# Kernel optimization log

Measured on AMD Instinct MI355X. Metric: run time of the kernel, lower is better.

The kernel has to match this reference:

```python
import jax, jax.numpy as jnp
import numpy as np

INPUT_DIM = 1024
EMBED_DIM = 1024
NUM_HEADS = 16
HEAD_DIM = EMBED_DIM // NUM_HEADS


def _xavier_uniform(key, shape):
    fan_in, fan_out = shape[1], shape[0]
    limit = float(np.sqrt(6.0 / (fan_in + fan_out)))
    return jax.random.uniform(key, shape, jnp.float32, -limit, limit)


def setup_inputs() -> dict:
    key = jax.random.key(0)
    kx, kqkv, ko = jax.random.split(key, 3)
    return {
        "x": jax.random.normal(kx, (2, 2048, INPUT_DIM), jnp.float32),
        "qkv_w": _xavier_uniform(kqkv, (3 * EMBED_DIM, INPUT_DIM)),
        "qkv_b": jnp.zeros((3 * EMBED_DIM,), jnp.float32),
        "o_w": _xavier_uniform(ko, (EMBED_DIM, INPUT_DIM)),
        "o_b": jnp.zeros((EMBED_DIM,), jnp.float32),
    }


def reference(x, qkv_w, qkv_b, o_w, o_b):
    B, S, _ = x.shape
    scale = HEAD_DIM ** -0.5
    # fused QKV projection: [B,S,3E]
    qkv = jnp.einsum('bsd,ed->bse', x, qkv_w) + qkv_b
    # [B,S,H,3Dh] -> [B,H,S,3Dh], then split into q,k,v
    qkv = qkv.reshape(B, S, NUM_HEADS, 3 * HEAD_DIM).transpose(0, 2, 1, 3)
    q, k, v = jnp.split(qkv, 3, axis=-1)
    # scaled dot-product attention
    scores = jnp.einsum('bhqd,bhkd->bhqk', q, k) * scale
    attn = jax.nn.softmax(scores, axis=-1)
    values = jnp.einsum('bhqk,bhkd->bhqd', attn, v)
    # [B,H,S,Dh] -> [B,S,E]
    values = values.transpose(0, 2, 1, 3).reshape(B, S, EMBED_DIM)
    return jnp.einsum('bse,oe->bso', values, o_w) + o_b
```

## Files before the change

### kernel.cpp

```cpp
#include <hip/hip_runtime.h>
#include <hip/hip_bf16.h>

typedef __bf16  bf16x8 __attribute__((ext_vector_type(8)));
typedef __bf16  bf16x4 __attribute__((ext_vector_type(4)));
typedef float   f32x4  __attribute__((ext_vector_type(4)));

#define LOG2E 1.44269504088896340736f

__device__ __forceinline__ void async_copy16(const void* g, void* l) {
  __builtin_amdgcn_global_load_lds(
      (const __attribute__((address_space(1))) unsigned int*)g,
      (__attribute__((address_space(3))) unsigned int*)l, 16, 0, 0);
}

#define C0 524288
#define C1 393216
#define C2 384
#define C3 131072
#define C4 128
#define CTOT (C0 + C1 + C2 + C3 + C4)
__global__ void convert_all(const void* __restrict__ x,  const void* __restrict__ qw,
                            const void* __restrict__ qb, const void* __restrict__ ow,
                            const void* __restrict__ ob,
                            __bf16* __restrict__ cx,  __bf16* __restrict__ cqw,
                            __bf16* __restrict__ cqb, __bf16* __restrict__ cow,
                            __bf16* __restrict__ cob, int* __restrict__ flag) {
  __shared__ int cnt;
  if (threadIdx.x == 0) cnt = 0;
  __syncthreads();
  unsigned int w = ((const unsigned int*)qw)[threadIdx.x];
  if (w & 0x4000u) atomicAdd(&cnt, 1);
  __syncthreads();
  const int f = (cnt > 16) ? 1 : 0;
  if (threadIdx.x == 0) *flag = f;

  int i = blockIdx.x * blockDim.x + threadIdx.x;
  const int stride = gridDim.x * blockDim.x;
  for (; i < CTOT; i += stride) {
    const void* s; __bf16* d; int off;
    if      (i < C0)                { s = x;  d = cx;  off = i; }
    else if (i < C0 + C1)           { s = qw; d = cqw; off = i - C0; }
    else if (i < C0 + C1 + C2)      { s = qb; d = cqb; off = i - C0 - C1; }
    else if (i < C0 + C1 + C2 + C3) { s = ow; d = cow; off = i - C0 - C1 - C2; }
    else                            { s = ob; d = cob; off = i - C0 - C1 - C2 - C3; }
    if (f) {
      const f32x4* sp = (const f32x4*)s;
      f32x4 a = sp[2 * off], b = sp[2 * off + 1];
      bf16x8 o;
      o[0] = (__bf16)a[0]; o[1] = (__bf16)a[1]; o[2] = (__bf16)a[2]; o[3] = (__bf16)a[3];
      o[4] = (__bf16)b[0]; o[5] = (__bf16)b[1]; o[6] = (__bf16)b[2]; o[7] = (__bf16)b[3];
      *(bf16x8*)&d[8 * off] = o;
    } else {
      *(bf16x8*)&d[8 * off] = ((const bf16x8*)s)[off];
    }
  }
}

template<int BN>
__global__ __launch_bounds__(256) void gemm_nt_bias(
    const __bf16* __restrict__ A,
    const __bf16* __restrict__ Bt,
    const __bf16* __restrict__ bias,
    __bf16* __restrict__ Cb,
    float* __restrict__ Cf,
    __bf16* __restrict__ vt,
    const int* __restrict__ flag,
    int M, int N, int K)
{
  constexpr int NI  = BN / 32;
  constexpr int NIB = BN / 32;
  __shared__ __align__(16) __bf16 As[128 * 64];
  __shared__ __align__(16) __bf16 Bs[BN * 64];

  const int tid  = threadIdx.x;
  const int lane = tid & 63;
  const int wave = tid >> 6;
  const int qd   = lane >> 4;
  const int ln   = lane & 15;
  const int m0 = blockIdx.y * 128;
  const int n0 = blockIdx.x * BN;
  const int wm = (wave >> 1) * 64;
  const int wn = (wave & 1) * (16 * NI);

  f32x4 acc[4][NI] = {};

  for (int kt = 0; kt < K; kt += 64) {
#pragma unroll
    for (int i = 0; i < 4; ++i) {
      int s = wave * 256 + i * 64 + lane;
      int r = s >> 3;
      int c = (s & 7) ^ (r & 7);
      async_copy16(A + (size_t)(m0 + r) * K + kt + c * 8, &As[(wave * 256 + i * 64) * 8]);
    }
#pragma unroll
    for (int i = 0; i < NIB; ++i) {
      int s = wave * (64 * NIB) + i * 64 + lane;
      int r = s >> 3;
      int c = (s & 7) ^ (r & 7);
      async_copy16(Bt + (size_t)(n0 + r) * K + kt + c * 8,
                   &Bs[(wave * (64 * NIB) + i * 64) * 8]);
    }
    __syncthreads();

#pragma unroll
    for (int kk = 0; kk < 2; ++kk) {
      bf16x8 af[4], bfr[NI];
#pragma unroll
      for (int t = 0; t < 4; ++t) {
        int ra = wm + t * 16 + ln;
        af[t] = *(const bf16x8*)&As[ra * 64 + (((kk * 4 + qd) ^ (ra & 7)) * 8)];
      }
#pragma unroll
      for (int t = 0; t < NI; ++t) {
        int rb = wn + t * 16 + ln;
        bfr[t] = *(const bf16x8*)&Bs[rb * 64 + (((kk * 4 + qd) ^ (rb & 7)) * 8)];
      }
#pragma unroll
      for (int mi = 0; mi < 4; ++mi)
#pragma unroll
        for (int ni = 0; ni < NI; ++ni)
          acc[mi][ni] = __builtin_amdgcn_mfma_f32_16x16x32_bf16(af[mi], bfr[ni], acc[mi][ni], 0, 0, 0);
    }
    __syncthreads();
  }

  const bool f32out = (Cf != nullptr) && (*flag != 0);
#pragma unroll
  for (int ni = 0; ni < NI; ++ni) {
    int cb0 = n0 + wn + ni * 16;
    int col = cb0 + ln;
    float bv = (float)bias[col];
    int grp = cb0 % 192;
    if (vt != nullptr && grp >= 128) {
      int hh = cb0 / 192;
      int d  = grp - 128 + ln;
#pragma unroll
      for (int mi = 0; mi < 4; ++mi) {
        int row0 = m0 + wm + mi * 16 + qd * 4;
        int bb = row0 >> 11, ss = row0 & 2047;
        bf16x4 w;
#pragma unroll
        for (int r = 0; r < 4; ++r) w[r] = (__bf16)(acc[mi][ni][r] + bv);
        *(bf16x4*)&vt[(((size_t)(bb * 16 + hh) * 64 + d) * 2048 + ss)] = w;
      }
    } else {
#pragma unroll
      for (int mi = 0; mi < 4; ++mi) {
#pragma unroll
        for (int r = 0; r < 4; ++r) {
          int row = m0 + wm + mi * 16 + qd * 4 + r;
          float v = acc[mi][ni][r] + bv;
          if (f32out) Cf[(size_t)row * N + col] = v;
          else        Cb[(size_t)row * N + col] = (__bf16)v;
        }
      }
    }
  }
}

#define PST 72
__global__ __launch_bounds__(256, 2) void attn_flash(
    const __bf16* __restrict__ qkv,
    const __bf16* __restrict__ vt,
    __bf16* __restrict__ vals)
{
  __shared__ __align__(16) unsigned char smem[69632];
  __bf16* Ks  = (__bf16*)smem;
  __bf16* VTs = (__bf16*)(smem + 16384);
  __bf16* Ps  = (__bf16*)(smem + 32768);

  const int tid  = threadIdx.x;
  const int lane = tid & 63;
  const int wave = tid >> 6;
  const int sh   = wave >> 1;
  const int wq   = wave & 1;
  const int qd   = lane >> 4;
  const int ln   = lane & 15;
  const int b  = blockIdx.y >> 4;
  const int h  = blockIdx.y & 15;
  const int q0 = blockIdx.x * 128;
  const __bf16* base = qkv + (size_t)b * 2048 * 3072 + h * 192;
  const __bf16* vbase = vt + (size_t)(b * 16 + h) * 64 * 2048;
  const int khalf = sh * 1024;

  bf16x8 qfr[4][2];
#pragma unroll
  for (int nt = 0; nt < 4; ++nt)
#pragma unroll
    for (int ks = 0; ks < 2; ++ks)
      qfr[nt][ks] = *(const bf16x8*)&base[(size_t)(q0 + wq * 64 + nt * 16 + ln) * 3072
                                          + ks * 32 + qd * 8];

  const float kScale = 0.125f * LOG2E;
  __bf16* P = Ps + wave * (64 * PST);

  f32x4 oaccT[4][4] = {};
  float lpart[4] = {0.f, 0.f, 0.f, 0.f};

  for (int it = 0; it < 16; ++it) {
    const int kt = khalf + it * 64;
    __syncthreads();

#pragma unroll
    for (int i = 0; i < 4; ++i) {
      int s  = wq * 256 + i * 64 + lane;
      int r  = s >> 3;
      int c  = (s & 7) ^ (r & 7);
      async_copy16(base + (size_t)(kt + r) * 3072 + 64 + c * 8,
                   &Ks[sh * 4096 + (wq * 256 + i * 64) * 8]);
      async_copy16(vbase + (size_t)r * 2048 + kt + c * 8,
                   &VTs[sh * 4096 + (wq * 256 + i * 64) * 8]);
    }
    __syncthreads();

    f32x4 sacc[4][4] = {};
#pragma unroll
    for (int ks = 0; ks < 2; ++ks) {
      bf16x8 kfr[4];
#pragma unroll
      for (int mi = 0; mi < 4; ++mi) {
        int row = mi * 16 + ln;
        kfr[mi] = *(const bf16x8*)&Ks[sh * 4096 + row * 64 + (((ks * 4 + qd) ^ (row & 7)) * 8)];
      }
#pragma unroll
      for (int nt = 0; nt < 4; ++nt)
#pragma unroll
        for (int mi = 0; mi < 4; ++mi)
          sacc[nt][mi] = __builtin_amdgcn_mfma_f32_16x16x32_bf16(kfr[mi], qfr[nt][ks], sacc[nt][mi], 0, 0, 0);
    }

#pragma unroll
    for (int nt = 0; nt < 4; ++nt) {
      float rs = 0.f;
#pragma unroll
      for (int mi = 0; mi < 4; ++mi) {
        float pv[4];
#pragma unroll
        for (int r = 0; r < 4; ++r) {
          pv[r] = __builtin_exp2f(sacc[nt][mi][r] * kScale);
          rs += pv[r];
        }
        bf16x4 w;
        w[0] = (__bf16)pv[0]; w[1] = (__bf16)pv[1];
        w[2] = (__bf16)pv[2]; w[3] = (__bf16)pv[3];
        *(bf16x4*)&P[(nt * 16 + ln) * PST + mi * 16 + qd * 4] = w;
      }
      lpart[nt] += rs;
    }

    asm volatile("s_waitcnt lgkmcnt(0)" ::: "memory");

#pragma unroll
    for (int ks = 0; ks < 2; ++ks) {
      bf16x8 vfr[4], pfr[4];
#pragma unroll
      for (int md = 0; md < 4; ++md) {
        int row = md * 16 + ln;
        vfr[md] = *(const bf16x8*)&VTs[sh * 4096 + row * 64 + (((ks * 4 + qd) ^ (row & 7)) * 8)];
      }
#pragma unroll
      for (int nt = 0; nt < 4; ++nt)
        pfr[nt] = *(const bf16x8*)&P[(nt * 16 + ln) * PST + ks * 32 + qd * 8];
#pragma unroll
      for (int nt = 0; nt < 4; ++nt)
#pragma unroll
        for (int md = 0; md < 4; ++md)
          oaccT[nt][md] = __builtin_amdgcn_mfma_f32_16x16x32_bf16(vfr[md], pfr[nt], oaccT[nt][md], 0, 0, 0);
    }
  }

  float lw[4];
#pragma unroll
  for (int nt = 0; nt < 4; ++nt) {
    float l = lpart[nt];
    l += __shfl_xor(l, 16);
    l += __shfl_xor(l, 32);
    lw[nt] = l;
  }
  __syncthreads();

  float* Sc = (float*)smem;
  float* Ls = (float*)(smem + 32768);

  if (sh == 0) {
#pragma unroll
    for (int nt = 0; nt < 4; ++nt) {
#pragma unroll
      for (int md = 0; md < 4; ++md)
        *(f32x4*)&Sc[((size_t)(wq * 64 + nt * 16 + ln)) * 64 + md * 16 + qd * 4] = oaccT[nt][md];
      if (qd == 0) Ls[wq * 64 + nt * 16 + ln] = lw[nt];
    }
  }
  __syncthreads();
  if (sh == 1) {
#pragma unroll
    for (int nt = 0; nt < 4; ++nt) {
      float il = 1.0f / (lw[nt] + Ls[wq * 64 + nt * 16 + ln]);
      int q = q0 + wq * 64 + nt * 16 + ln;
      __bf16* o = vals + ((size_t)b * 2048 + q) * 1024 + h * 64;
#pragma unroll
      for (int md = 0; md < 4; ++md) {
        f32x4 part = *(const f32x4*)&Sc[((size_t)(wq * 64 + nt * 16 + ln)) * 64 + md * 16 + qd * 4];
        bf16x4 w;
#pragma unroll
        for (int r = 0; r < 4; ++r)
          w[r] = (__bf16)((oaccT[nt][md][r] + part[r]) * il);
        *(bf16x4*)&o[md * 16 + qd * 4] = w;
      }
    }
  }
}

extern "C" void kernel_launch(void* const* d_in, const int* in_sizes, int n_in,
                              void* d_out, int out_size, void* d_ws, size_t ws_size,
                              hipStream_t stream) {
  __bf16* ws    = (__bf16*)d_ws;
  __bf16* qkv   = ws;
  __bf16* vals  = qkv   + (size_t)4096 * 3072;
  __bf16* cx    = vals  + (size_t)4096 * 1024;
  __bf16* cqkvw = cx    + (size_t)4096 * 1024;
  __bf16* cow   = cqkvw + (size_t)3072 * 1024;
  __bf16* cqkvb = cow   + (size_t)1024 * 1024;
  __bf16* cob   = cqkvb + 4096;
  int*    flag  = (int*)(cob + 4096);
  __bf16* vT    = (__bf16*)(flag + 64);

  dim3 blk(256);

  convert_all<<<1024, 256, 0, stream>>>(d_in[0], d_in[1], d_in[2], d_in[3], d_in[4],
                                        cx, cqkvw, cqkvb, cow, cob, flag);

  gemm_nt_bias<128><<<dim3(3072 / 128, 4096 / 128), blk, 0, stream>>>(
      cx, cqkvw, cqkvb, qkv, nullptr, vT, flag, 4096, 3072, 1024);

  attn_flash<<<dim3(2048 / 128, 32), blk, 0, stream>>>(qkv, vT, vals);

  gemm_nt_bias<64><<<dim3(1024 / 64, 4096 / 128), blk, 0, stream>>>(
      vals, cow, cob, (__bf16*)d_out, (float*)d_out, nullptr, flag, 4096, 1024, 1024);
}
```

Before: 196.7 us.

## Load K and V fragments directly from global into registers, drop LDS staging

The attention kernel stops staging K and V^T tiles in shared memory through async copies with block barriers. Each wave now loads its K and V MFMA fragments straight from global memory into registers, prefetching the next K tile one iteration ahead. The score computation is split into two halves to limit live accumulator registers. This removes the per-iteration __syncthreads pairs and shrinks LDS, but every wave now fetches K/V separately, and the larger register footprint with relaxed launch bounds can lower occupancy.

```diff
diff --git a/kernel.cpp b/kernel.cpp
--- a/kernel.cpp
+++ b/kernel.cpp
@@ -159,15 +159,13 @@
 }
 
 #define PST 72
-__global__ __launch_bounds__(256, 2) void attn_flash(
+__global__ __launch_bounds__(256) void attn_flash(
     const __bf16* __restrict__ qkv,
     const __bf16* __restrict__ vt,
     __bf16* __restrict__ vals)
 {
-  __shared__ __align__(16) unsigned char smem[69632];
-  __bf16* Ks  = (__bf16*)smem;
-  __bf16* VTs = (__bf16*)(smem + 16384);
-  __bf16* Ps  = (__bf16*)(smem + 32768);
+  __shared__ __align__(16) unsigned char smem[36864];
+  __bf16* Ps = (__bf16*)smem;
 
   const int tid  = threadIdx.x;
   const int lane = tid & 63;
@@ -197,67 +195,71 @@
   f32x4 oaccT[4][4] = {};
   float lpart[4] = {0.f, 0.f, 0.f, 0.f};
 
+  bf16x8 kcur[2][4], knext[2][4];
+#pragma unroll
+  for (int ks = 0; ks < 2; ++ks)
+#pragma unroll
+    for (int mi = 0; mi < 4; ++mi)
+      kcur[ks][mi] = *(const bf16x8*)&base[(size_t)(khalf + mi * 16 + ln) * 3072
+                                           + 64 + ks * 32 + qd * 8];
+
   for (int it = 0; it < 16; ++it) {
-    const int kt = khalf + it * 64;
-    __syncthreads();
-
-#pragma unroll
-    for (int i = 0; i < 4; ++i) {
-      int s  = wq * 256 + i * 64 + lane;
-      int r  = s >> 3;
-      int c  = (s & 7) ^ (r & 7);
-      async_copy16(base + (size_t)(kt + r) * 3072 + 64 + c * 8,
-                   &Ks[sh * 4096 + (wq * 256 + i * 64) * 8]);
-      async_copy16(vbase + (size_t)r * 2048 + kt + c * 8,
-                   &VTs[sh * 4096 + (wq * 256 + i * 64) * 8]);
-    }
-    __syncthreads();
-
-    f32x4 sacc[4][4] = {};
+    const int kt  = khalf + it * 64;
+    const int ktn = khalf + (((it + 1) & 15) << 6);
+
+#pragma unroll
+    for (int ks = 0; ks < 2; ++ks)
+#pragma unroll
+      for (int mi = 0; mi < 4; ++mi)
+        knext[ks][mi] = *(const bf16x8*)&base[(size_t)(ktn + mi * 16 + ln) * 3072
+                                              + 64 + ks * 32 + qd * 8];
+
+    bf16x8 vcur[2][4];
+#pragma unroll
+    for (int ks = 0; ks < 2; ++ks)
+#pragma unroll
+      for (int md = 0; md < 4; ++md)
+        vcur[ks][md] = *(const bf16x8*)&vbase[(size_t)(md * 16 + ln) * 2048
+                                              + kt + ks * 32 + qd * 8];
+
+#pragma unroll
+    for (int nth = 0; nth < 2; ++nth) {
+      f32x4 sacc[2][4] = {};
+#pragma unroll
+      for (int ks = 0; ks < 2; ++ks)
+#pragma unroll
+        for (int n2 = 0; n2 < 2; ++n2)
+#pragma unroll
+          for (int mi = 0; mi < 4; ++mi)
+            sacc[n2][mi] = __builtin_amdgcn_mfma_f32_16x16x32_bf16(
+                kcur[ks][mi], qfr[nth * 2 + n2][ks], sacc[n2][mi], 0, 0, 0);
+
+#pragma unroll
+      for (int n2 = 0; n2 < 2; ++n2) {
+        const int nt = nth * 2 + n2;
+        float rs = 0.f;
+#pragma unroll
+        for (int mi = 0; mi < 4; ++mi) {
+          float pv[4];
+#pragma unroll
+          for (int r = 0; r < 4; ++r) {
+            pv[r] = __builtin_exp2f(sacc[n2][mi][r] * kScale);
+            rs += pv[r];
+          }
+          bf16x4 w;
+          w[0] = (__bf16)pv[0]; w[1] = (__bf16)pv[1];
+          w[2] = (__bf16)pv[2]; w[3] = (__bf16)pv[3];
+          *(bf16x4*)&P[(nt * 16 + ln) * PST + mi * 16 + qd * 4] = w;
+        }
+        lpart[nt] += rs;
+      }
+    }
+
+    asm volatile("s_waitcnt lgkmcnt(0)" ::: "memory");
+
 #pragma unroll
     for (int ks = 0; ks < 2; ++ks) {
-      bf16x8 kfr[4];
-#pragma unroll
-      for (int mi = 0; mi < 4; ++mi) {
-        int row = mi * 16 + ln;
-        kfr[mi] = *(const bf16x8*)&Ks[sh * 4096 + row * 64 + (((ks * 4 + qd) ^ (row & 7)) * 8)];
-      }
-#pragma unroll
-      for (int nt = 0; nt < 4; ++nt)
-#pragma unroll
-        for (int mi = 0; mi < 4; ++mi)
-          sacc[nt][mi] = __builtin_amdgcn_mfma_f32_16x16x32_bf16(kfr[mi], qfr[nt][ks], sacc[nt][mi], 0, 0, 0);
-    }
-
-#pragma unroll
-    for (int nt = 0; nt < 4; ++nt) {
-      float rs = 0.f;
-#pragma unroll
-      for (int mi = 0; mi < 4; ++mi) {
-        float pv[4];
-#pragma unroll
-        for (int r = 0; r < 4; ++r) {
-          pv[r] = __builtin_exp2f(sacc[nt][mi][r] * kScale);
-          rs += pv[r];
-        }
-        bf16x4 w;
-        w[0] = (__bf16)pv[0]; w[1] = (__bf16)pv[1];
-        w[2] = (__bf16)pv[2]; w[3] = (__bf16)pv[3];
-        *(bf16x4*)&P[(nt * 16 + ln) * PST + mi * 16 + qd * 4] = w;
-      }
-      lpart[nt] += rs;
-    }
-
-    asm volatile("s_waitcnt lgkmcnt(0)" ::: "memory");
-
-#pragma unroll
-    for (int ks = 0; ks < 2; ++ks) {
-      bf16x8 vfr[4], pfr[4];
-#pragma unroll
-      for (int md = 0; md < 4; ++md) {
-        int row = md * 16 + ln;
-        vfr[md] = *(const bf16x8*)&VTs[sh * 4096 + row * 64 + (((ks * 4 + qd) ^ (row & 7)) * 8)];
-      }
+      bf16x8 pfr[4];
 #pragma unroll
       for (int nt = 0; nt < 4; ++nt)
         pfr[nt] = *(const bf16x8*)&P[(nt * 16 + ln) * PST + ks * 32 + qd * 8];
@@ -265,8 +267,15 @@
       for (int nt = 0; nt < 4; ++nt)
 #pragma unroll
         for (int md = 0; md < 4; ++md)
-          oaccT[nt][md] = __builtin_amdgcn_mfma_f32_16x16x32_bf16(vfr[md], pfr[nt], oaccT[nt][md], 0, 0, 0);
-    }
+          oaccT[nt][md] = __builtin_amdgcn_mfma_f32_16x16x32_bf16(
+              vcur[ks][md], pfr[nt], oaccT[nt][md], 0, 0, 0);
+    }
+
+#pragma unroll
+    for (int ks = 0; ks < 2; ++ks)
+#pragma unroll
+      for (int mi = 0; mi < 4; ++mi)
+        kcur[ks][mi] = knext[ks][mi];
   }
 
   float lw[4];
```

New measurement: 208.9 us. +6.2%, slower.

## Double-buffer GEMM LDS tiles with K-step 32 and prefetch the next tile

Applied to the files above, without the earlier changes.

The NT GEMM used a single 64-wide K tile in LDS with two barriers per step. It now keeps two 32-wide K buffers and issues the async global-to-LDS load for the next K slice right after the barrier, before computing on the current slice. The aim is to overlap global memory latency with MFMA work and drop one barrier per iteration. In exchange there are twice as many loop iterations and barriers over K, less MFMA work per barrier, and a narrower 4-chunk XOR swizzle that may cause more LDS bank conflicts.

```diff
diff --git a/kernel.cpp b/kernel.cpp
--- a/kernel.cpp
+++ b/kernel.cpp
@@ -68,9 +68,9 @@
     int M, int N, int K)
 {
   constexpr int NI  = BN / 32;
-  constexpr int NIB = BN / 32;
-  __shared__ __align__(16) __bf16 As[128 * 64];
-  __shared__ __align__(16) __bf16 Bs[BN * 64];
+  constexpr int BCH = (BN * 4) / 256;
+  __shared__ __align__(16) __bf16 As[2][128 * 32];
+  __shared__ __align__(16) __bf16 Bs[2][BN * 32];
 
   const int tid  = threadIdx.x;
   const int lane = tid & 63;
@@ -84,44 +84,48 @@
 
   f32x4 acc[4][NI] = {};
 
-  for (int kt = 0; kt < K; kt += 64) {
-#pragma unroll
-    for (int i = 0; i < 4; ++i) {
-      int s = wave * 256 + i * 64 + lane;
-      int r = s >> 3;
-      int c = (s & 7) ^ (r & 7);
-      async_copy16(A + (size_t)(m0 + r) * K + kt + c * 8, &As[(wave * 256 + i * 64) * 8]);
-    }
-#pragma unroll
-    for (int i = 0; i < NIB; ++i) {
-      int s = wave * (64 * NIB) + i * 64 + lane;
-      int r = s >> 3;
-      int c = (s & 7) ^ (r & 7);
+  auto stage = [&](int kt, int buf) {
+#pragma unroll
+    for (int i = 0; i < 2; ++i) {
+      int s = wave * 128 + i * 64 + lane;
+      int r = s >> 2;
+      int c = (s & 3) ^ (r & 3);
+      async_copy16(A + (size_t)(m0 + r) * K + kt + c * 8,
+                   &As[buf][(wave * 128 + i * 64) * 8]);
+    }
+#pragma unroll
+    for (int i = 0; i < BCH; ++i) {
+      int s = wave * (64 * BCH) + i * 64 + lane;
+      int r = s >> 2;
+      int c = (s & 3) ^ (r & 3);
       async_copy16(Bt + (size_t)(n0 + r) * K + kt + c * 8,
-                   &Bs[(wave * (64 * NIB) + i * 64) * 8]);
-    }
+                   &Bs[buf][(wave * (64 * BCH) + i * 64) * 8]);
+    }
+  };
+
+  stage(0, 0);
+  const int NIT = K / 32;
+  for (int ki = 0; ki < NIT; ++ki) {
+    const int cur = ki & 1;
     __syncthreads();
-
-#pragma unroll
-    for (int kk = 0; kk < 2; ++kk) {
-      bf16x8 af[4], bfr[NI];
-#pragma unroll
-      for (int t = 0; t < 4; ++t) {
-        int ra = wm + t * 16 + ln;
-        af[t] = *(const bf16x8*)&As[ra * 64 + (((kk * 4 + qd) ^ (ra & 7)) * 8)];
-      }
-#pragma unroll
-      for (int t = 0; t < NI; ++t) {
-        int rb = wn + t * 16 + ln;
-        bfr[t] = *(const bf16x8*)&Bs[rb * 64 + (((kk * 4 + qd) ^ (rb & 7)) * 8)];
-      }
-#pragma unroll
-      for (int mi = 0; mi < 4; ++mi)
-#pragma unroll
-        for (int ni = 0; ni < NI; ++ni)
-          acc[mi][ni] = __builtin_amdgcn_mfma_f32_16x16x32_bf16(af[mi], bfr[ni], acc[mi][ni], 0, 0, 0);
-    }
-    __syncthreads();
+    if (ki + 1 < NIT) stage((ki + 1) * 32, cur ^ 1);
+
+    bf16x8 af[4], bfr[NI];
+#pragma unroll
+    for (int t = 0; t < 4; ++t) {
+      int ra = wm + t * 16 + ln;
+      af[t] = *(const bf16x8*)&As[cur][ra * 32 + ((qd ^ (ra & 3)) * 8)];
+    }
+#pragma unroll
+    for (int t = 0; t < NI; ++t) {
+      int rb = wn + t * 16 + ln;
+      bfr[t] = *(const bf16x8*)&Bs[cur][rb * 32 + ((qd ^ (rb & 3)) * 8)];
+    }
+#pragma unroll
+    for (int mi = 0; mi < 4; ++mi)
+#pragma unroll
+      for (int ni = 0; ni < NI; ++ni)
+        acc[mi][ni] = __builtin_amdgcn_mfma_f32_16x16x32_bf16(af[mi], bfr[ni], acc[mi][ni], 0, 0, 0);
   }
 
   const bool f32out = (Cf != nullptr) && (*flag != 0);
```

Measured after the change: 201.5 us. 2.5% more time.
